# Performance work log

Hardware: AMD Instinct MI355X
Metric: run time of the kernel (lower is better)

Reference implementation:

```python
import jax, jax.numpy as jnp
import numpy as np

TSHAPE = (256, 256, 1024)
RANK = 32


def setup_inputs() -> dict:
    key = jax.random.key(0)
    k0, k1, k2 = jax.random.split(key, 3)
    # Nonnegative factor matrices, columns normalized to sum to 1 (as in NTF.__init__
    # via reinit_mode + norm_mode_within_factor).
    W0 = jax.random.uniform(k0, (TSHAPE[0], RANK), dtype=jnp.float32)
    W1 = jax.random.uniform(k1, (TSHAPE[1], RANK), dtype=jnp.float32)
    W2 = jax.random.uniform(k2, (TSHAPE[2], RANK), dtype=jnp.float32)
    W0 = W0 / W0.sum(axis=0)
    W1 = W1 / W1.sum(axis=0)
    W2 = W2 / W2.sum(axis=0)
    return {"W0": W0, "W1": W1, "W2": W2}


def reference(W0, W1, W2):
    # CP reconstruction: outer_prod(modes).sum(axis=-1)
    # == sum_r W0[:, r] (x) W1[:, r] (x) W2[:, r]  -> shape TSHAPE
    # einsum fuses the rank reduction, avoiding the (i, j, k, r) intermediate.
    return jnp.einsum("ir,jr,kr->ijk", W0, W1, W2)
```

## Files before the change

kernel.cpp:

```cpp
#include <hip/hip_runtime.h>


constexpr int I_DIM  = 256;
constexpr int J_DIM  = 256;
constexpr int K_DIM  = 1024;
constexpr int RNK    = 32;
constexpr int JSEG   = 64;
constexpr int KSPLIT = 2;
constexpr int KCHUNK = K_DIM / KSPLIT;

typedef float f32x2 __attribute__((ext_vector_type(2)));

__global__ void transpose_w2(const float* __restrict__ W2, float* __restrict__ W2T) {
    int idx = blockIdx.x * 256 + threadIdx.x;
    int r = idx >> 10;
    int k = idx & (K_DIM - 1);
    W2T[r * K_DIM + k] = W2[k * RNK + r];
}

__global__ void precompute_c(const float* __restrict__ W0, const float* __restrict__ W1,
                             float* __restrict__ C) {
    int idx = blockIdx.x * 256 + threadIdx.x;
    int r = idx & 31;
    int j = (idx >> 5) & 255;
    int i = idx >> 13;
    C[idx] = W0[i * RNK + r] * W1[j * RNK + r];
}

__global__ __launch_bounds__(256, 4) void cp_recon_f2(const float* __restrict__ C,
                                                      const float* __restrict__ W2T,
                                                      float* __restrict__ out) {
    const int b     = blockIdx.x;
    const int khalf = b & (KSPLIT - 1);
    const int jseg  = (b >> 1) & 3;
    const int i     = b >> 3;
    const int jbase = jseg * JSEG;
    const int k     = khalf * KCHUNK + threadIdx.x * 2;

    float2 w[RNK];
#pragma unroll
    for (int r = 0; r < RNK; ++r)
        w[r] = *reinterpret_cast<const float2*>(&W2T[r * K_DIM + k]);

    const float* __restrict__ crow = C + (size_t)(i * J_DIM + jbase) * RNK;
    float* __restrict__ obase = out + (size_t)(i * J_DIM + jbase) * K_DIM + k;

#pragma unroll 2
    for (int jj = 0; jj < JSEG; ++jj) {
        const float* __restrict__ cj = crow + jj * RNK;
        float ax = 0.f, ay = 0.f;
#pragma unroll
        for (int r = 0; r < RNK; ++r) {
            float s = cj[r];
            ax = fmaf(s, w[r].x, ax);
            ay = fmaf(s, w[r].y, ay);
        }
        f32x2 t = { ax, ay };
        *reinterpret_cast<f32x2*>(obase + (size_t)jj * K_DIM) = t;
    }
}

constexpr int JT = 8;
__global__ __launch_bounds__(256, 4) void cp_recon_d(const float* __restrict__ W0,
                                                     const float* __restrict__ W1,
                                                     const float* __restrict__ W2,
                                                     float* __restrict__ out) {
    __shared__ __align__(16) float c[JT][RNK];
    const int i     = blockIdx.x >> 5;
    const int jbase = (blockIdx.x & 31) * JT;
    const int tid   = threadIdx.x;

    if (tid < JT * RNK) {
        int jj = tid >> 5;
        int r  = tid & 31;
        c[jj][r] = W0[i * RNK + r] * W1[(jbase + jj) * RNK + r];
    }
    __syncthreads();

    const int k = tid * 4;
    float4 acc[JT];
#pragma unroll
    for (int jj = 0; jj < JT; ++jj) acc[jj] = make_float4(0.f, 0.f, 0.f, 0.f);

    for (int rc = 0; rc < RNK; rc += 4) {
        float4 row[4];
#pragma unroll
        for (int q = 0; q < 4; ++q)
            row[q] = *reinterpret_cast<const float4*>(&W2[(k + q) * RNK + rc]);
#pragma unroll
        for (int jj = 0; jj < JT; ++jj) {
            float4 c4 = *reinterpret_cast<const float4*>(&c[jj][rc]);
            acc[jj].x = fmaf(c4.x, row[0].x, fmaf(c4.y, row[0].y, fmaf(c4.z, row[0].z, fmaf(c4.w, row[0].w, acc[jj].x))));
            acc[jj].y = fmaf(c4.x, row[1].x, fmaf(c4.y, row[1].y, fmaf(c4.z, row[1].z, fmaf(c4.w, row[1].w, acc[jj].y))));
            acc[jj].z = fmaf(c4.x, row[2].x, fmaf(c4.y, row[2].y, fmaf(c4.z, row[2].z, fmaf(c4.w, row[2].w, acc[jj].z))));
            acc[jj].w = fmaf(c4.x, row[3].x, fmaf(c4.y, row[3].y, fmaf(c4.z, row[3].z, fmaf(c4.w, row[3].w, acc[jj].w))));
        }
    }
#pragma unroll
    for (int jj = 0; jj < JT; ++jj) {
        int o = (i * J_DIM + jbase + jj) * K_DIM + k;
        *reinterpret_cast<float4*>(&out[o]) = acc[jj];
    }
}

extern "C" void kernel_launch(void* const* d_in, const int* in_sizes, int n_in,
                              void* d_out, int out_size, void* d_ws, size_t ws_size,
                              hipStream_t stream) {
    const float* W0 = (const float*)d_in[0];
    const float* W1 = (const float*)d_in[1];
    const float* W2 = (const float*)d_in[2];
    float* out = (float*)d_out;

    const size_t w2t_bytes = (size_t)RNK * K_DIM * sizeof(float);
    const size_t c_bytes   = (size_t)I_DIM * J_DIM * RNK * sizeof(float);

    if (ws_size >= w2t_bytes + c_bytes) {
        float* W2T  = (float*)d_ws;
        float* Cbuf = (float*)((char*)d_ws + w2t_bytes);
        transpose_w2<<<(RNK * K_DIM) / 256, 256, 0, stream>>>(W2, W2T);
        precompute_c<<<(I_DIM * J_DIM * RNK) / 256, 256, 0, stream>>>(W0, W1, Cbuf);
        const int grid = I_DIM * (J_DIM / JSEG) * KSPLIT;
        cp_recon_f2<<<grid, 256, 0, stream>>>(Cbuf, W2T, out);
    } else {
        cp_recon_d<<<I_DIM * (J_DIM / JT), 256, 0, stream>>>(W0, W1, W2, out);
    }
}
```

Before: 73.03 us.

## Use one output per thread with four-way K split and XCD-aware block remap

Each thread in the main reconstruction kernel now computes one k value instead of two, and K is split four ways, so the grid doubles. This halves per-thread register use for the W2 slice and allows eight blocks per CU. Block indices are remapped so consecutive logical work items go to the same XCD, which is meant to improve L2 reuse of the C rows. In exchange, each C row is read from global/cache twice as often per output, and stores become scalar rather than 2-wide.

Result: slower. 256.8 us (+251.6%).

```diff
diff --git a/kernel.cpp b/kernel.cpp
--- a/kernel.cpp
+++ b/kernel.cpp
@@ -6,10 +6,9 @@
 constexpr int K_DIM  = 1024;
 constexpr int RNK    = 32;
 constexpr int JSEG   = 64;
-constexpr int KSPLIT = 2;
-constexpr int KCHUNK = K_DIM / KSPLIT;
-
-typedef float f32x2 __attribute__((ext_vector_type(2)));
+constexpr int KQ     = 4;
+constexpr int KCHUNK = K_DIM / KQ;
+constexpr int NXCD   = 8;
 
 __global__ void transpose_w2(const float* __restrict__ W2, float* __restrict__ W2T) {
     int idx = blockIdx.x * 256 + threadIdx.x;
@@ -27,20 +26,21 @@
     C[idx] = W0[i * RNK + r] * W1[j * RNK + r];
 }
 
-__global__ __launch_bounds__(256, 4) void cp_recon_f2(const float* __restrict__ C,
+__global__ __launch_bounds__(256, 8) void cp_recon_f1(const float* __restrict__ C,
                                                       const float* __restrict__ W2T,
                                                       float* __restrict__ out) {
-    const int b     = blockIdx.x;
-    const int khalf = b & (KSPLIT - 1);
-    const int jseg  = (b >> 1) & 3;
-    const int i     = b >> 3;
+    const int b    = blockIdx.x;
+    const int w_id = (b & (NXCD - 1)) * (4096 / NXCD) + (b >> 3);
+    const int i    = w_id >> 4;
+    const int jseg = (w_id >> 2) & 3;
+    const int kq   = w_id & (KQ - 1);
     const int jbase = jseg * JSEG;
-    const int k     = khalf * KCHUNK + threadIdx.x * 2;
+    const int k     = kq * KCHUNK + threadIdx.x;
 
-    float2 w[RNK];
+    float w[RNK];
 #pragma unroll
     for (int r = 0; r < RNK; ++r)
-        w[r] = *reinterpret_cast<const float2*>(&W2T[r * K_DIM + k]);
+        w[r] = W2T[r * K_DIM + k];
 
     const float* __restrict__ crow = C + (size_t)(i * J_DIM + jbase) * RNK;
     float* __restrict__ obase = out + (size_t)(i * J_DIM + jbase) * K_DIM + k;
@@ -48,15 +48,11 @@
 #pragma unroll 2
     for (int jj = 0; jj < JSEG; ++jj) {
         const float* __restrict__ cj = crow + jj * RNK;
-        float ax = 0.f, ay = 0.f;
+        float acc = 0.f;
 #pragma unroll
-        for (int r = 0; r < RNK; ++r) {
-            float s = cj[r];
-            ax = fmaf(s, w[r].x, ax);
-            ay = fmaf(s, w[r].y, ay);
-        }
-        f32x2 t = { ax, ay };
-        *reinterpret_cast<f32x2*>(obase + (size_t)jj * K_DIM) = t;
+        for (int r = 0; r < RNK; ++r)
+            acc = fmaf(cj[r], w[r], acc);
+        obase[(size_t)jj * K_DIM] = acc;
     }
 }
 
@@ -119,8 +115,8 @@
         float* Cbuf = (float*)((char*)d_ws + w2t_bytes);
         transpose_w2<<<(RNK * K_DIM) / 256, 256, 0, stream>>>(W2, W2T);
         precompute_c<<<(I_DIM * J_DIM * RNK) / 256, 256, 0, stream>>>(W0, W1, Cbuf);
-        const int grid = I_DIM * (J_DIM / JSEG) * KSPLIT;
-        cp_recon_f2<<<grid, 256, 0, stream>>>(Cbuf, W2T, out);
+        const int grid = I_DIM * (J_DIM / JSEG) * KQ;
+        cp_recon_f1<<<grid, 256, 0, stream>>>(Cbuf, W2T, out);
     } else {
         cp_recon_d<<<I_DIM * (J_DIM / JT), 256, 0, stream>>>(W0, W1, W2, out);
     }
```
